# Performance work log

Measured on AMD Instinct MI355X. Metric: run time of the kernel, lower is better.

## Reference

```python
import jax, jax.numpy as jnp
import numpy as np

NUM_C = 100
DIM_S = 128
SIZE_M = 64
EMB = 128
MAX_CODE_LEN = 128
NODE_COUNT = 10000
PATH_COUNT = 10000
B, L = 16, 128


def setup_inputs() -> dict:
    key = jax.random.key(0)
    ks = jax.random.split(key, 24)
    def nrm(k, shape, fan):
        return jax.random.normal(k, shape, jnp.float32) * np.float32(np.sqrt(2.0 / fan))
    code = jax.random.randint(ks[0], (B, L, NUM_C * 2 + MAX_CODE_LEN * 3), 0, 10000)
    q = jax.random.randint(ks[1], (B, L), 0, NUM_C)
    r = jax.random.randint(ks[2], (B, L), 0, 2 * NUM_C)
    return {
        "code": code, "q": q, "r": r,
        "embed_nodes": nrm(ks[3], (NODE_COUNT + 2, EMB), EMB),
        "embed_paths": nrm(ks[4], (PATH_COUNT + 2, EMB), EMB),
        "W_pt": nrm(ks[5], (3 * EMB, 3 * EMB), 3 * EMB), "b_pt": jnp.zeros((3 * EMB,), jnp.float32),
        "W_att": nrm(ks[6], (3 * EMB, 1), 3 * EMB), "b_att": jnp.zeros((1,), jnp.float32),
        "k_emb": nrm(ks[7], (NUM_C + 1, DIM_S), DIM_S),
        "Mk": nrm(ks[8], (SIZE_M, DIM_S), DIM_S),
        "Mv0": nrm(ks[9], (SIZE_M, DIM_S), DIM_S),
        "v_emb": nrm(ks[10], (NUM_C * 2 + 2, DIM_S), DIM_S),
        "W_e": nrm(ks[11], (4 * DIM_S, DIM_S), 4 * DIM_S), "b_e": jnp.zeros((DIM_S,), jnp.float32),
        "W_a": nrm(ks[12], (4 * DIM_S, DIM_S), 4 * DIM_S), "b_a": jnp.zeros((DIM_S,), jnp.float32),
        "W_f": nrm(ks[13], (2 * DIM_S, DIM_S), 2 * DIM_S), "b_f": jnp.zeros((DIM_S,), jnp.float32),
        "W_p": nrm(ks[14], (DIM_S, 10), DIM_S), "b_p": jnp.zeros((10,), jnp.float32),
    }


def reference(code, q, r, embed_nodes, embed_paths, W_pt, b_pt, W_att, b_att,
              k_emb, Mk, Mv0, v_emb, W_e, b_e, W_a, b_a, W_f, b_f, W_p, b_p):
    bsz = code.shape[0]
    k = k_emb[q]                                    # [B,L,D]
    vr = v_emb[r]                                   # [B,L,D]
    # code2vec path triples: [B,L,MAX_CODE_LEN,3] = (start, path, end)
    c2v = code[:, :, NUM_C * 2:].reshape(bsz, code.shape[1], MAX_CODE_LEN, 3)
    full = jnp.concatenate([embed_nodes[c2v[..., 0]],
                            embed_nodes[c2v[..., 2]],
                            embed_paths[c2v[..., 1]]], axis=3)   # [B,L,P,3E]
    tr = jnp.tanh(full @ W_pt + b_pt)
    cw = tr @ W_att + b_att                          # [B,L,P,1]
    attn = jax.nn.softmax(cw, axis=1)                # faithful: softmax over seq dim (dim=1)
    code_vec = jnp.sum(full * attn, axis=2)          # [B,L,3E]
    v = jnp.concatenate([vr, code_vec], axis=2)      # [B,L,4D]
    w = jax.nn.softmax(k @ Mk.T, axis=-1)            # [B,L,M]
    e = jax.nn.sigmoid(v @ W_e + b_e)                # [B,L,D]
    a = jnp.tanh(v @ W_a + b_a)                      # [B,L,D]
    Mvt0 = jnp.broadcast_to(Mv0, (bsz,) + Mv0.shape) # [B,M,D]

    def step(Mvt, inp):
        et, at, wt = inp                             # [B,D],[B,D],[B,M]
        read = jnp.einsum('bm,bmd->bd', wt, Mvt)     # read pre-update memory (Mv[:, :-1])
        Mvt = Mvt * (1.0 - wt[:, :, None] * et[:, None, :]) + wt[:, :, None] * at[:, None, :]
        return Mvt, read

    _, reads = jax.lax.scan(step, Mvt0,
                            (e.transpose(1, 0, 2), a.transpose(1, 0, 2), w.transpose(1, 0, 2)))
    read = reads.transpose(1, 0, 2)                  # [B,L,D]
    f = jnp.tanh(jnp.concatenate([read, k], axis=-1) @ W_f + b_f)
    # dropout is identity in eval mode
    return jax.nn.sigmoid(f @ W_p + b_p)             # [B,L,10]
```

## Files before the change

### kernel.cpp

```cpp
#include <hip/hip_runtime.h>


typedef unsigned char u8;
typedef unsigned short u16;
typedef unsigned int u32;
typedef __attribute__((ext_vector_type(8))) short short8;
typedef __attribute__((ext_vector_type(4))) float f32x4;
typedef __attribute__((ext_vector_type(2))) float f32x2;

#define DEV __device__ __forceinline__
#define LOG2E 1.4426950408889634f
#define KSCALE 2.8853900817779268f

DEV u16 f2b(float f) {
    union { float f; u32 i; } v; v.f = f;
    u32 x = v.i;
    u32 r = (x + 0x7FFFu + ((x >> 16) & 1u)) >> 16;
    return (u16)r;
}
DEV float nexp(float x) { return __builtin_amdgcn_exp2f(x * LOG2E); }
DEV float nrcp(float x) { return __builtin_amdgcn_rcpf(x); }
DEV float fast_tanh(float x) {
    return 1.f - 2.f * nrcp(1.f + __builtin_amdgcn_exp2f(x * (2.f * LOG2E)));
}
DEV float sigmoidf_(float x) { return nrcp(1.f + __builtin_amdgcn_exp2f(-x * LOG2E)); }
DEV f32x2 d8(u32 x, bool hi) {
    return hi ? __builtin_amdgcn_cvt_pk_f32_fp8((int)x, true)
              : __builtin_amdgcn_cvt_pk_f32_fp8((int)x, false);
}
DEV u8 e8(float x) {
    return (u8)(__builtin_amdgcn_cvt_pk_fp8_f32(x, x, 0, false) & 0xFF);
}

__global__ void k_conv(const float* __restrict__ EN, const float* __restrict__ EP,
                       const float* __restrict__ Wpt, const float* __restrict__ We,
                       const float* __restrict__ Wa, const float* __restrict__ Wf,
                       const float* __restrict__ Wp,
                       const float* __restrict__ Kemb, const float* __restrict__ Mk,
                       u16* __restrict__ ENb, u16* __restrict__ EPb,
                       u8* __restrict__ EN8, u8* __restrict__ EP8,
                       u16* __restrict__ Wt, u16* __restrict__ WeaT,
                       u16* __restrict__ WfT, u16* __restrict__ WpT,
                       float* __restrict__ wsmall) {
    if (blockIdx.x >= 2048) {
        int wv = threadIdx.x >> 6, lane = threadIdx.x & 63;
        int row = (blockIdx.x - 2048) * 4 + wv;
        if (row >= 101) return;
        float lg = 0.f;
        for (int k = 0; k < 128; k += 8) {
            float mk8[8];
#pragma unroll
            for (int u = 0; u < 8; u++) mk8[u] = Mk[lane * 128 + k + u];
#pragma unroll
            for (int u = 0; u < 8; u++) lg = fmaf(Kemb[row * 128 + k + u], mk8[u], lg);
        }
        float mx = lg;
#pragma unroll
        for (int off = 32; off; off >>= 1) mx = fmaxf(mx, __shfl_xor(mx, off, 64));
        float ex = nexp(lg - mx);
        float sum = ex;
#pragma unroll
        for (int off = 32; off; off >>= 1) sum += __shfl_xor(sum, off, 64);
        wsmall[row * 64 + lane] = ex * nrcp(sum);
        return;
    }
    const int NEH = 10002 * 64;
    const int T0 = 2 * NEH;
    const int T1 = T0 + 147456;
    const int T2 = T1 + 131072;
    const int T3 = T2 + 32768;
    const int T4 = T3 + 2048;
    for (int i = blockIdx.x * blockDim.x + threadIdx.x; i < T4; i += 2048 * blockDim.x) {
        if (i < NEH) {
            float a = EN[2 * i], b = EN[2 * i + 1];
            ((u32*)ENb)[i] = ((u32)f2b(b) << 16) | f2b(a);
            ((u16*)EN8)[i] = (u16)__builtin_amdgcn_cvt_pk_fp8_f32(a, b, 0, false);
        } else if (i < T0) {
            int j = i - NEH;
            float a = EP[2 * j], b = EP[2 * j + 1];
            ((u32*)EPb)[j] = ((u32)f2b(b) << 16) | f2b(a);
            ((u16*)EP8)[j] = (u16)__builtin_amdgcn_cvt_pk_fp8_f32(a, b, 0, false);
        } else if (i < T1) {
            int w = i - T0;  u32 n = (u32)w / 384u, k = (u32)w % 384u;
            Wt[w] = f2b(Wpt[k * 384 + n]);
        } else if (i < T2) {
            int w = i - T1;  int n = w >> 9, k = w & 511;
            WeaT[w] = f2b((n < 128) ? We[k * 128 + n] : Wa[k * 128 + (n - 128)]);
        } else if (i < T3) {
            int w = i - T2;  int n = w >> 8, k = w & 255;
            WfT[w] = f2b(Wf[k * 128 + n]);
        } else {
            int w = i - T3;  int n = w >> 7, k = w & 127;
            WpT[w] = (n < 10) ? f2b(Wp[k * 10 + n]) : (u16)0;
        }
    }
}

__global__ void k_preM(const u16* __restrict__ ENb, const u16* __restrict__ EPb,
                       const u16* __restrict__ Wt, const float* __restrict__ bpt,
                       u8* __restrict__ PS8, u8* __restrict__ PE8, u8* __restrict__ PP8) {
    int which = blockIdx.y;
    int r0 = blockIdx.x * 32;
    int wv = threadIdx.x >> 6, lane = threadIdx.x & 63;
    int m = lane & 15, quad = lane >> 4;
    const u16* A = (which == 2) ? EPb : ENb;
    int koff = which * 128;
    u8* dst = (which == 0) ? PS8 : (which == 1) ? PE8 : PP8;

    short8 a[2][4];
#pragma unroll
    for (int rt = 0; rt < 2; rt++) {
        const short8* ap = (const short8*)(A + (r0 + rt * 16 + m) * 128 + quad * 8);
#pragma unroll
        for (int kc = 0; kc < 4; kc++) a[rt][kc] = ap[kc * 4];
    }

    for (int nt = 0; nt < 6; nt++) {
        int n0 = wv * 96 + nt * 16;
        const short8* bp = (const short8*)(Wt + (n0 + m) * 384 + koff + quad * 8);
        short8 b0 = bp[0], b1 = bp[4], b2 = bp[8], b3 = bp[12];
        int col = n0 + m;
        float bias = (which == 2) ? bpt[col] : 0.f;
#pragma unroll
        for (int rt = 0; rt < 2; rt++) {
            f32x4 acc = {0.f, 0.f, 0.f, 0.f};
            acc = __builtin_amdgcn_mfma_f32_16x16x32_bf16(a[rt][0], b0, acc, 0, 0, 0);
            acc = __builtin_amdgcn_mfma_f32_16x16x32_bf16(a[rt][1], b1, acc, 0, 0, 0);
            acc = __builtin_amdgcn_mfma_f32_16x16x32_bf16(a[rt][2], b2, acc, 0, 0, 0);
            acc = __builtin_amdgcn_mfma_f32_16x16x32_bf16(a[rt][3], b3, acc, 0, 0, 0);
#pragma unroll
            for (int reg = 0; reg < 4; reg++) {
                int row = r0 + rt * 16 + quad * 4 + reg;
                if (row < 10002) dst[row * 384 + col] = e8((acc[reg] + bias) * KSCALE);
            }
        }
    }
}

__global__ void k_cw(const int* __restrict__ code,
                     const u8* __restrict__ PS8, const u8* __restrict__ PE8,
                     const u8* __restrict__ PP8, const float* __restrict__ Watt,
                     float* __restrict__ cw) {
    int wv = threadIdx.x >> 6, lane = threadIdx.x & 63;
    int g = lane >> 4, gl = lane & 15;
    int t0 = (blockIdx.x * 4 + wv) * 8;
    int b = t0 >> 14;
    int rem = t0 & 16383;
    int l = rem >> 7, p0 = rem & 127;

    const int* c = code + ((b * 128 + l) * 584 + 200 + 3 * p0);
    int si[8], pi[8], ei[8];
#pragma unroll
    for (int i = 0; i < 8; i++) {
        si[i] = __builtin_amdgcn_readfirstlane(c[3 * i]);
        pi[i] = __builtin_amdgcn_readfirstlane(c[3 * i + 1]);
        ei[i] = __builtin_amdgcn_readfirstlane(c[3 * i + 2]);
    }

    float w24[24];
    const float4* wp = (const float4*)(Watt + gl * 24);
#pragma unroll
    for (int u = 0; u < 6; u++) {
        float4 f = wp[u];
        w24[4 * u + 0] = -2.f * f.x; w24[4 * u + 1] = -2.f * f.y;
        w24[4 * u + 2] = -2.f * f.z; w24[4 * u + 3] = -2.f * f.w;
    }

    float res[2];
#pragma unroll
    for (int batch = 0; batch < 2; batch++) {
        int i = batch * 4 + g;
        const uint2* bs = (const uint2*)(PS8 + si[i] * 384 + gl * 24);
        const uint2* be = (const uint2*)(PE8 + ei[i] * 384 + gl * 24);
        const uint2* bq = (const uint2*)(PP8 + pi[i] * 384 + gl * 24);
        uint2 s0 = bs[0], s1 = bs[1], s2 = bs[2];
        uint2 e0 = be[0], e1 = be[1], e2 = be[2];
        uint2 q0 = bq[0], q1 = bq[1], q2 = bq[2];

        float acc = 0.f;
        u32 sv[6] = { s0.x, s0.y, s1.x, s1.y, s2.x, s2.y };
        u32 ev[6] = { e0.x, e0.y, e1.x, e1.y, e2.x, e2.y };
        u32 qv[6] = { q0.x, q0.y, q1.x, q1.y, q2.x, q2.y };
#pragma unroll
        for (int u = 0; u < 6; u++) {
            f32x2 zl = d8(sv[u], false) + d8(ev[u], false) + d8(qv[u], false);
            f32x2 zh = d8(sv[u], true)  + d8(ev[u], true)  + d8(qv[u], true);
            acc = fmaf(nrcp(1.f + __builtin_amdgcn_exp2f(zl.x)), w24[4 * u + 0], acc);
            acc = fmaf(nrcp(1.f + __builtin_amdgcn_exp2f(zl.y)), w24[4 * u + 1], acc);
            acc = fmaf(nrcp(1.f + __builtin_amdgcn_exp2f(zh.x)), w24[4 * u + 2], acc);
            acc = fmaf(nrcp(1.f + __builtin_amdgcn_exp2f(zh.y)), w24[4 * u + 3], acc);
        }
        acc += __shfl_xor(acc, 1, 64);
        acc += __shfl_xor(acc, 2, 64);
        acc += __shfl_xor(acc, 4, 64);
        acc += __shfl_xor(acc, 8, 64);
        res[batch] = acc;
    }
    if (gl == 0) {
        cw[(b * 128 + p0 + g) * 128 + l] = res[0];
        cw[(b * 128 + p0 + 4 + g) * 128 + l] = res[1];
    }
}

__global__ void k_sm(const float* __restrict__ cw, float* __restrict__ attn) {
    int b = blockIdx.x >> 3, p0 = (blockIdx.x & 7) * 16;
    int tid = threadIdx.x;
    int wv = tid >> 6, lane = tid & 63;
    __shared__ float tile[16][128];
    __shared__ float atile[128][17];
    for (int idx = tid; idx < 2048; idx += 256) {
        int pp = idx >> 7, l = idx & 127;
        tile[pp][l] = cw[(b * 128 + p0 + pp) * 128 + l];
    }
    __syncthreads();
#pragma unroll
    for (int pl = 0; pl < 4; pl++) {
        int pp = wv * 4 + pl;
        float x0 = tile[pp][lane], x1 = tile[pp][64 + lane];
        float mx = fmaxf(x0, x1);
#pragma unroll
        for (int off = 32; off; off >>= 1) mx = fmaxf(mx, __shfl_xor(mx, off, 64));
        float e0 = nexp(x0 - mx), e1 = nexp(x1 - mx);
        float sum = e0 + e1;
#pragma unroll
        for (int off = 32; off; off >>= 1) sum += __shfl_xor(sum, off, 64);
        float inv = nrcp(sum);
        atile[lane][pp] = e0 * inv;
        atile[64 + lane][pp] = e1 * inv;
    }
    __syncthreads();
    for (int idx = tid; idx < 2048; idx += 256) {
        int l = idx >> 4, pp = idx & 15;
        attn[(b * 128 + l) * 128 + p0 + pp] = atile[l][pp];
    }
}

__global__ void k_cv(const int* __restrict__ code, const float* __restrict__ attn,
                     const u8* __restrict__ EN8, const u8* __restrict__ EP8,
                     const int* __restrict__ rr, const int* __restrict__ qq,
                     const float* __restrict__ Vemb, const float* __restrict__ Kemb,
                     u16* __restrict__ vA, u16* __restrict__ fA) {
    int row = blockIdx.x;
    int tid = threadIdx.x;
    int wv = tid >> 6, lane = tid & 63;
    __shared__ int si[128], ei[128], pi[128];
    __shared__ float at[128];
    __shared__ float part[4][3][128];
    if (tid < 128) {
        const int* c = code + (row * 584 + 200);
        si[tid] = c[3 * tid]; pi[tid] = c[3 * tid + 1]; ei[tid] = c[3 * tid + 2];
        at[tid] = attn[row * 128 + tid];
    }
    if (tid < 128) {
        vA[row * 512 + tid] = f2b(Vemb[rr[row] * 128 + tid]);
    } else {
        int t2 = tid - 128;
        fA[row * 256 + 128 + t2] = f2b(Kemb[qq[row] * 128 + t2]);
    }
    __syncthreads();
    float a0 = 0.f, a1 = 0.f, b0 = 0.f, b1 = 0.f, c0 = 0.f, c1 = 0.f;
    int o = 2 * lane;

    u32 cur[6];
    {
        int p = wv, p2 = wv + 4;
        cur[0] = *(const u16*)(EN8 + si[p] * 128 + o);
        cur[1] = *(const u16*)(EN8 + ei[p] * 128 + o);
        cur[2] = *(const u16*)(EP8 + pi[p] * 128 + o);
        cur[3] = *(const u16*)(EN8 + si[p2] * 128 + o);
        cur[4] = *(const u16*)(EN8 + ei[p2] * 128 + o);
        cur[5] = *(const u16*)(EP8 + pi[p2] * 128 + o);
    }
#pragma unroll
    for (int it = 0; it < 16; it++) {
        int p = wv + it * 8;
        u32 nxt[6];
        if (it < 15) {
            int pn = p + 8, pn2 = p + 12;
            nxt[0] = *(const u16*)(EN8 + si[pn] * 128 + o);
            nxt[1] = *(const u16*)(EN8 + ei[pn] * 128 + o);
            nxt[2] = *(const u16*)(EP8 + pi[pn] * 128 + o);
            nxt[3] = *(const u16*)(EN8 + si[pn2] * 128 + o);
            nxt[4] = *(const u16*)(EN8 + ei[pn2] * 128 + o);
            nxt[5] = *(const u16*)(EP8 + pi[pn2] * 128 + o);
        }
        float w = at[p], w2 = at[p + 4];
        f32x2 fs = d8(cur[0], false), fe = d8(cur[1], false), fp = d8(cur[2], false);
        f32x2 gs = d8(cur[3], false), ge = d8(cur[4], false), gp = d8(cur[5], false);
        a0 = fmaf(w, fs.x, a0); a1 = fmaf(w, fs.y, a1);
        b0 = fmaf(w, fe.x, b0); b1 = fmaf(w, fe.y, b1);
        c0 = fmaf(w, fp.x, c0); c1 = fmaf(w, fp.y, c1);
        a0 = fmaf(w2, gs.x, a0); a1 = fmaf(w2, gs.y, a1);
        b0 = fmaf(w2, ge.x, b0); b1 = fmaf(w2, ge.y, b1);
        c0 = fmaf(w2, gp.x, c0); c1 = fmaf(w2, gp.y, c1);
        if (it < 15) {
#pragma unroll
            for (int z = 0; z < 6; z++) cur[z] = nxt[z];
        }
    }
    part[wv][0][2 * lane] = a0; part[wv][0][2 * lane + 1] = a1;
    part[wv][1][2 * lane] = b0; part[wv][1][2 * lane + 1] = b1;
    part[wv][2][2 * lane] = c0; part[wv][2][2 * lane + 1] = c1;
    __syncthreads();
    u16* vrow = vA + row * 512 + 128;
    for (int idx = tid; idx < 384; idx += 256) {
        int tbl = idx >> 7, col = idx & 127;
        vrow[idx] = f2b(part[0][tbl][col] + part[1][tbl][col] + part[2][tbl][col] + part[3][tbl][col]);
    }
}

__global__ void k_eawM(const u16* __restrict__ vA, const u16* __restrict__ WeaT,
                       const float* __restrict__ be, const float* __restrict__ ba,
                       float* __restrict__ eb, float* __restrict__ ab) {
    int rt = blockIdx.x >> 2, cg = blockIdx.x & 3;
    int wv = threadIdx.x >> 6, lane = threadIdx.x & 63;
    int ct = cg * 4 + wv;
    int m = lane & 15, quad = lane >> 4;
    const short8* ap = (const short8*)(vA + (rt * 16 + m) * 512 + quad * 8);
    const short8* bp = (const short8*)(WeaT + (ct * 16 + m) * 512 + quad * 8);
    f32x4 acc = {0.f, 0.f, 0.f, 0.f};
#pragma unroll
    for (int kc = 0; kc < 16; kc++)
        acc = __builtin_amdgcn_mfma_f32_16x16x32_bf16(ap[kc * 4], bp[kc * 4], acc, 0, 0, 0);
    int col = ct * 16 + m;
    bool isA = col >= 128;
    int c2 = isA ? col - 128 : col;
    float bias = isA ? ba[c2] : be[c2];
#pragma unroll
    for (int reg = 0; reg < 4; reg++) {
        int row = rt * 16 + quad * 4 + reg;
        float val = acc[reg] + bias;
        if (isA) ab[row * 128 + c2] = fast_tanh(val);
        else     eb[row * 128 + c2] = sigmoidf_(val);
    }
}

__global__ void k_scan(const float* __restrict__ Mv0, const float* __restrict__ eb,
                       const float* __restrict__ ab, const float* __restrict__ wsmall,
                       const int* __restrict__ qq, u16* __restrict__ fA) {
    int b = blockIdx.x >> 4, dblk = blockIdx.x & 15;
    int lane = threadIdx.x;
    int s = lane >> 3, dlo = lane & 7;
    int d = dblk * 8 + dlo;

    __shared__ float wsm[101 * 64];
    __shared__ float el[128][8];
    __shared__ float al[128][8];
    __shared__ int ql[128];

    for (int i = lane; i < 101 * 64; i += 64) wsm[i] = wsmall[i];
    for (int i = lane; i < 1024; i += 64) {
        int t = i >> 3, dl = i & 7;
        el[t][dl] = eb[(b * 128 + t) * 128 + dblk * 8 + dl];
        al[t][dl] = ab[(b * 128 + t) * 128 + dblk * 8 + dl];
    }
    for (int i = lane; i < 128; i += 64) ql[i] = qq[b * 128 + i];
    __syncthreads();

    float mv[8];
#pragma unroll
    for (int q = 0; q < 8; q++) mv[q] = Mv0[(s * 8 + q) * 128 + d];

    u16* fout = fA + (b * 128) * 256 + d;

    int qt = ql[0];
    const float4* wr = (const float4*)(wsm + qt * 64 + s * 8);
    float4 w0 = wr[0], w1 = wr[1];
    float ecur = el[0][dlo], acur = al[0][dlo];

    for (int t = 0; t < 128; t++) {
        int tn = (t < 127) ? t + 1 : 127;
        int qn = ql[tn];
        const float4* wrn = (const float4*)(wsm + qn * 64 + s * 8);
        float4 nw0 = wrn[0], nw1 = wrn[1];
        float en = el[tn][dlo], an = al[tn][dlo];

        float w[8] = { w0.x, w0.y, w0.z, w0.w, w1.x, w1.y, w1.z, w1.w };
        float rd = 0.f;
#pragma unroll
        for (int q = 0; q < 8; q++) {
            rd = fmaf(w[q], mv[q], rd);
            mv[q] = fmaf(w[q], fmaf(-mv[q], ecur, acur), mv[q]);
        }
        rd += __shfl_xor(rd, 8, 64);
        rd += __shfl_xor(rd, 16, 64);
        rd += __shfl_xor(rd, 32, 64);
        if (s == 0) fout[t * 256] = f2b(rd);

        ecur = en; acur = an; w0 = nw0; w1 = nw1;
    }
}

__global__ void k_outfin(const u16* __restrict__ fA, const u16* __restrict__ WfT,
                         const float* __restrict__ bfp, const u16* __restrict__ WpT,
                         const float* __restrict__ bp, float* __restrict__ out) {
    int rt = blockIdx.x;
    int wv = threadIdx.x >> 6, lane = threadIdx.x & 63;
    int m = lane & 15, quad = lane >> 4;
    __shared__ u16 ftile[16][128];

    const short8* ap = (const short8*)(fA + (rt * 16 + m) * 256 + quad * 8);
    const short8* bpw = (const short8*)(WfT + (wv * 16 + m) * 256 + quad * 8);
    f32x4 acc = {0.f, 0.f, 0.f, 0.f};
#pragma unroll
    for (int kc = 0; kc < 8; kc++)
        acc = __builtin_amdgcn_mfma_f32_16x16x32_bf16(ap[kc * 4], bpw[kc * 4], acc, 0, 0, 0);
    int col = wv * 16 + m;
    float bias = bfp[col];
#pragma unroll
    for (int reg = 0; reg < 4; reg++)
        ftile[quad * 4 + reg][col] = f2b(fast_tanh(acc[reg] + bias));
    __syncthreads();

    if (wv == 0) {
        f32x4 facc = {0.f, 0.f, 0.f, 0.f};
#pragma unroll
        for (int kc = 0; kc < 4; kc++) {
            short8 af = *(const short8*)(&ftile[m][kc * 32 + quad * 8]);
            short8 bf = *(const short8*)(WpT + m * 128 + kc * 32 + quad * 8);
            facc = __builtin_amdgcn_mfma_f32_16x16x32_bf16(af, bf, facc, 0, 0, 0);
        }
        if (m < 10) {
            float bias2 = bp[m];
#pragma unroll
            for (int reg = 0; reg < 4; reg++) {
                int row = rt * 16 + quad * 4 + reg;
                out[row * 10 + m] = sigmoidf_(facc[reg] + bias2);
            }
        }
    }
}

extern "C" void kernel_launch(void* const* d_in, const int* in_sizes, int n_in,
                              void* d_out, int out_size, void* d_ws, size_t ws_size,
                              hipStream_t stream) {
    const int*   code = (const int*)d_in[0];
    const int*   q    = (const int*)d_in[1];
    const int*   r    = (const int*)d_in[2];
    const float* EN   = (const float*)d_in[3];
    const float* EP   = (const float*)d_in[4];
    const float* Wpt  = (const float*)d_in[5];
    const float* bpt  = (const float*)d_in[6];
    const float* Watt = (const float*)d_in[7];
    const float* Kemb = (const float*)d_in[9];
    const float* Mk   = (const float*)d_in[10];
    const float* Mv0  = (const float*)d_in[11];
    const float* Vemb = (const float*)d_in[12];
    const float* We   = (const float*)d_in[13];
    const float* be   = (const float*)d_in[14];
    const float* Wa   = (const float*)d_in[15];
    const float* ba   = (const float*)d_in[16];
    const float* Wf   = (const float*)d_in[17];
    const float* bf_  = (const float*)d_in[18];
    const float* Wp   = (const float*)d_in[19];
    const float* bp   = (const float*)d_in[20];

    char* ws = (char*)d_ws;
    size_t off = 0;
    auto alloc = [&](size_t bytes) { void* p = ws + off; off = (off + bytes + 255) & ~255UL; return p; };
    u8*    PS8    = (u8*)alloc(10002UL * 384);
    u8*    PE8    = (u8*)alloc(10002UL * 384);
    u8*    PP8    = (u8*)alloc(10002UL * 384);
    u16*   ENb    = (u16*)alloc(10016UL * 128 * 2);
    u16*   EPb    = (u16*)alloc(10016UL * 128 * 2);
    u8*    EN8    = (u8*)alloc(10002UL * 128);
    u8*    EP8    = (u8*)alloc(10002UL * 128);
    u16*   Wt     = (u16*)alloc(384UL * 384 * 2);
    u16*   WeaT   = (u16*)alloc(256UL * 512 * 2);
    u16*   WfT    = (u16*)alloc(128UL * 256 * 2);
    u16*   WpT    = (u16*)alloc(16UL * 128 * 2);
    float* cw     = (float*)alloc(16UL * 128 * 128 * 4);
    float* attn   = (float*)alloc(16UL * 128 * 128 * 4);
    u16*   vA     = (u16*)alloc(2048UL * 512 * 2);
    u16*   fA     = (u16*)alloc(2048UL * 256 * 2);
    float* eb     = (float*)alloc(2048UL * 128 * 4);
    float* ab     = (float*)alloc(2048UL * 128 * 4);
    float* wsmall = (float*)alloc(101UL * 64 * 4);

    k_conv<<<2048 + 26, 256, 0, stream>>>(EN, EP, Wpt, We, Wa, Wf, Wp, Kemb, Mk,
                                          ENb, EPb, EN8, EP8, Wt, WeaT, WfT, WpT, wsmall);
    k_preM<<<dim3(313, 3), 256, 0, stream>>>(ENb, EPb, Wt, bpt, PS8, PE8, PP8);
    k_cw<<<8192, 256, 0, stream>>>(code, PS8, PE8, PP8, Watt, cw);
    k_sm<<<128, 256, 0, stream>>>(cw, attn);
    k_cv<<<2048, 256, 0, stream>>>(code, attn, EN8, EP8, r, q, Vemb, Kemb, vA, fA);
    k_eawM<<<512, 256, 0, stream>>>(vA, WeaT, be, ba, eb, ab);
    k_scan<<<256, 64, 0, stream>>>(Mv0, eb, ab, wsmall, q, fA);
    k_outfin<<<128, 512, 0, stream>>>(fA, WfT, bf_, WpT, bp, (float*)d_out);
}
```

Baseline: 226.2 us.

## Fuse code-attention logits and seq-dim softmax into one kernel with prefetching

Merges the logit kernel and the softmax-over-sequence kernel so that each block computes all 128 sequence logits for one (batch, path) pair, keeps them in shared memory and applies the softmax directly. This removes the intermediate cw buffer round-trip and one kernel launch. The gather loop now software-pipelines the next row's embedding loads while the current row is being computed. In exchange, the code indices are loaded per lane without readfirstlane, so each 16-lane group does its own scattered loads, and the block needs extra barriers for the reduction.

```diff
diff --git a/kernel.cpp b/kernel.cpp
--- a/kernel.cpp
+++ b/kernel.cpp
@@ -137,25 +137,16 @@
     }
 }
 
-__global__ void k_cw(const int* __restrict__ code,
-                     const u8* __restrict__ PS8, const u8* __restrict__ PE8,
-                     const u8* __restrict__ PP8, const float* __restrict__ Watt,
-                     float* __restrict__ cw) {
-    int wv = threadIdx.x >> 6, lane = threadIdx.x & 63;
-    int g = lane >> 4, gl = lane & 15;
-    int t0 = (blockIdx.x * 4 + wv) * 8;
-    int b = t0 >> 14;
-    int rem = t0 & 16383;
-    int l = rem >> 7, p0 = rem & 127;
-
-    const int* c = code + ((b * 128 + l) * 584 + 200 + 3 * p0);
-    int si[8], pi[8], ei[8];
-#pragma unroll
-    for (int i = 0; i < 8; i++) {
-        si[i] = __builtin_amdgcn_readfirstlane(c[3 * i]);
-        pi[i] = __builtin_amdgcn_readfirstlane(c[3 * i + 1]);
-        ei[i] = __builtin_amdgcn_readfirstlane(c[3 * i + 2]);
-    }
+__global__ void k_cwsm(const int* __restrict__ code,
+                       const u8* __restrict__ PS8, const u8* __restrict__ PE8,
+                       const u8* __restrict__ PP8, const float* __restrict__ Watt,
+                       float* __restrict__ attn) {
+    int bp = blockIdx.x;
+    int b = bp >> 7, p = bp & 127;
+    int tid = threadIdx.x;
+    int g = tid >> 4, gl = tid & 15;
+    __shared__ float lgs[128];
+    __shared__ float redm[4], reds[4];
 
     float w24[24];
     const float4* wp = (const float4*)(Watt + gl * 24);
@@ -166,21 +157,37 @@
         w24[4 * u + 2] = -2.f * f.z; w24[4 * u + 3] = -2.f * f.w;
     }
 
-    float res[2];
-#pragma unroll
-    for (int batch = 0; batch < 2; batch++) {
-        int i = batch * 4 + g;
-        const uint2* bs = (const uint2*)(PS8 + si[i] * 384 + gl * 24);
-        const uint2* be = (const uint2*)(PE8 + ei[i] * 384 + gl * 24);
-        const uint2* bq = (const uint2*)(PP8 + pi[i] * 384 + gl * 24);
-        uint2 s0 = bs[0], s1 = bs[1], s2 = bs[2];
-        uint2 e0 = be[0], e1 = be[1], e2 = be[2];
-        uint2 q0 = bq[0], q1 = bq[1], q2 = bq[2];
-
+    int si[8], pi[8], ei[8];
+#pragma unroll
+    for (int it = 0; it < 8; it++) {
+        const int* c = code + ((b * 128 + g + it * 16) * 584 + 200 + 3 * p);
+        si[it] = c[0]; pi[it] = c[1]; ei[it] = c[2];
+    }
+
+    uint2 cs0, cs1, cs2, ce0, ce1, ce2, cq0, cq1, cq2;
+    {
+        const uint2* bs = (const uint2*)(PS8 + si[0] * 384 + gl * 24);
+        const uint2* be = (const uint2*)(PE8 + ei[0] * 384 + gl * 24);
+        const uint2* bq = (const uint2*)(PP8 + pi[0] * 384 + gl * 24);
+        cs0 = bs[0]; cs1 = bs[1]; cs2 = bs[2];
+        ce0 = be[0]; ce1 = be[1]; ce2 = be[2];
+        cq0 = bq[0]; cq1 = bq[1]; cq2 = bq[2];
+    }
+#pragma unroll
+    for (int it = 0; it < 8; it++) {
+        uint2 ns0, ns1, ns2, ne0, ne1, ne2, nq0, nq1, nq2;
+        if (it < 7) {
+            const uint2* bs = (const uint2*)(PS8 + si[it + 1] * 384 + gl * 24);
+            const uint2* be = (const uint2*)(PE8 + ei[it + 1] * 384 + gl * 24);
+            const uint2* bq = (const uint2*)(PP8 + pi[it + 1] * 384 + gl * 24);
+            ns0 = bs[0]; ns1 = bs[1]; ns2 = bs[2];
+            ne0 = be[0]; ne1 = be[1]; ne2 = be[2];
+            nq0 = bq[0]; nq1 = bq[1]; nq2 = bq[2];
+        }
+        u32 sv[6] = { cs0.x, cs0.y, cs1.x, cs1.y, cs2.x, cs2.y };
+        u32 ev[6] = { ce0.x, ce0.y, ce1.x, ce1.y, ce2.x, ce2.y };
+        u32 qv[6] = { cq0.x, cq0.y, cq1.x, cq1.y, cq2.x, cq2.y };
         float acc = 0.f;
-        u32 sv[6] = { s0.x, s0.y, s1.x, s1.y, s2.x, s2.y };
-        u32 ev[6] = { e0.x, e0.y, e1.x, e1.y, e2.x, e2.y };
-        u32 qv[6] = { q0.x, q0.y, q1.x, q1.y, q2.x, q2.y };
 #pragma unroll
         for (int u = 0; u < 6; u++) {
             f32x2 zl = d8(sv[u], false) + d8(ev[u], false) + d8(qv[u], false);
@@ -194,45 +201,31 @@
         acc += __shfl_xor(acc, 2, 64);
         acc += __shfl_xor(acc, 4, 64);
         acc += __shfl_xor(acc, 8, 64);
-        res[batch] = acc;
-    }
-    if (gl == 0) {
-        cw[(b * 128 + p0 + g) * 128 + l] = res[0];
-        cw[(b * 128 + p0 + 4 + g) * 128 + l] = res[1];
-    }
-}
-
-__global__ void k_sm(const float* __restrict__ cw, float* __restrict__ attn) {
-    int b = blockIdx.x >> 3, p0 = (blockIdx.x & 7) * 16;
-    int tid = threadIdx.x;
-    int wv = tid >> 6, lane = tid & 63;
-    __shared__ float tile[16][128];
-    __shared__ float atile[128][17];
-    for (int idx = tid; idx < 2048; idx += 256) {
-        int pp = idx >> 7, l = idx & 127;
-        tile[pp][l] = cw[(b * 128 + p0 + pp) * 128 + l];
-    }
-    __syncthreads();
-#pragma unroll
-    for (int pl = 0; pl < 4; pl++) {
-        int pp = wv * 4 + pl;
-        float x0 = tile[pp][lane], x1 = tile[pp][64 + lane];
-        float mx = fmaxf(x0, x1);
-#pragma unroll
-        for (int off = 32; off; off >>= 1) mx = fmaxf(mx, __shfl_xor(mx, off, 64));
-        float e0 = nexp(x0 - mx), e1 = nexp(x1 - mx);
-        float sum = e0 + e1;
-#pragma unroll
-        for (int off = 32; off; off >>= 1) sum += __shfl_xor(sum, off, 64);
-        float inv = nrcp(sum);
-        atile[lane][pp] = e0 * inv;
-        atile[64 + lane][pp] = e1 * inv;
-    }
-    __syncthreads();
-    for (int idx = tid; idx < 2048; idx += 256) {
-        int l = idx >> 4, pp = idx & 15;
-        attn[(b * 128 + l) * 128 + p0 + pp] = atile[l][pp];
-    }
+        if (gl == 0) lgs[g + it * 16] = acc;
+        if (it < 7) {
+            cs0 = ns0; cs1 = ns1; cs2 = ns2;
+            ce0 = ne0; ce1 = ne1; ce2 = ne2;
+            cq0 = nq0; cq1 = nq1; cq2 = nq2;
+        }
+    }
+    __syncthreads();
+
+    int lane = tid & 63, wvi = tid >> 6;
+    float x = (tid < 128) ? lgs[tid] : -1e30f;
+    float mx = x;
+#pragma unroll
+    for (int off = 32; off; off >>= 1) mx = fmaxf(mx, __shfl_xor(mx, off, 64));
+    if (lane == 0) redm[wvi] = mx;
+    __syncthreads();
+    mx = fmaxf(redm[0], redm[1]);
+    float ex = nexp(x - mx);
+    float sum = ex;
+#pragma unroll
+    for (int off = 32; off; off >>= 1) sum += __shfl_xor(sum, off, 64);
+    if (lane == 0) reds[wvi] = sum;
+    __syncthreads();
+    float inv = nrcp(reds[0] + reds[1]);
+    if (tid < 128) attn[(b * 128 + tid) * 128 + p] = ex * inv;
 }
 
 __global__ void k_cv(const int* __restrict__ code, const float* __restrict__ attn,
@@ -469,7 +462,6 @@
     u16*   WeaT   = (u16*)alloc(256UL * 512 * 2);
     u16*   WfT    = (u16*)alloc(128UL * 256 * 2);
     u16*   WpT    = (u16*)alloc(16UL * 128 * 2);
-    float* cw     = (float*)alloc(16UL * 128 * 128 * 4);
     float* attn   = (float*)alloc(16UL * 128 * 128 * 4);
     u16*   vA     = (u16*)alloc(2048UL * 512 * 2);
     u16*   fA     = (u16*)alloc(2048UL * 256 * 2);
@@ -480,8 +472,7 @@
     k_conv<<<2048 + 26, 256, 0, stream>>>(EN, EP, Wpt, We, Wa, Wf, Wp, Kemb, Mk,
                                           ENb, EPb, EN8, EP8, Wt, WeaT, WfT, WpT, wsmall);
     k_preM<<<dim3(313, 3), 256, 0, stream>>>(ENb, EPb, Wt, bpt, PS8, PE8, PP8);
-    k_cw<<<8192, 256, 0, stream>>>(code, PS8, PE8, PP8, Watt, cw);
-    k_sm<<<128, 256, 0, stream>>>(cw, attn);
+    k_cwsm<<<2048, 256, 0, stream>>>(code, PS8, PE8, PP8, Watt, attn);
     k_cv<<<2048, 256, 0, stream>>>(code, attn, EN8, EP8, r, q, Vemb, Kemb, vA, fA);
     k_eawM<<<512, 256, 0, stream>>>(vA, WeaT, be, ba, eb, ab);
     k_scan<<<256, 64, 0, stream>>>(Mv0, eb, ab, wsmall, q, fA);
```

Result: no change. 224.0 us (-1.0%).
